# Kernel optimization log

Measured on AMD Instinct MI355X. Metric: run time of the kernel, lower is better.

Reference implementation:

```python
import jax, jax.numpy as jnp
import numpy as np

VOCAB, EMBED, HIDDEN, NCLS, PAD = 50257, 512, 1024, 4, 0

def setup_inputs() -> dict:
    key = jax.random.key(0)
    k1, k2, k3, k4, k5, k6 = jax.random.split(key, 6)
    emb = jax.random.uniform(k1, (VOCAB, EMBED), jnp.float32, -0.1, 0.1)
    emb = emb.at[PAD].set(0.0)
    W = jax.random.normal(k2, (HIDDEN, EMBED), jnp.float32) * (2.0 / (EMBED + HIDDEN)) ** 0.5
    b_w = jnp.zeros((HIDDEN,), jnp.float32)
    U = jax.random.normal(k3, (HIDDEN, HIDDEN), jnp.float32) * (1.0 / HIDDEN) ** 0.5
    V = jax.random.normal(k4, (NCLS, HIDDEN), jnp.float32) * (2.0 / (HIDDEN + NCLS)) ** 0.5
    b_v = jnp.zeros((NCLS,), jnp.float32)
    x = jax.random.randint(k5, (64, 512), 0, VOCAB, jnp.int32)
    return {"x": x, "emb": emb, "W": W, "b_w": b_w, "U": U, "V": V, "b_v": b_v}

def reference(x, emb, W, b_w, U, V, b_v):
    # x: [B, S] int tokens. Dropouts are identity (eval mode).
    embedded = emb[x]                      # [B, S, E]
    # Precompute Wx for all timesteps in one GEMM: [B, S, H]
    wx = jnp.einsum('bse,he->bsh', embedded, W) + b_w
    B = x.shape[0]
    h0 = jnp.zeros((B, W.shape[0]), embedded.dtype)

    def step(h, wx_t):
        h = jnp.tanh(wx_t + h @ U.T)       # [B, H]
        return h, None

    h_final, _ = jax.lax.scan(step, h0, jnp.swapaxes(wx, 0, 1))  # scan over S
    return h_final @ V.T + b_v             # [B, NCLS]
```

## Files before the change

### kernel.cpp

```cpp
#include <hip/hip_runtime.h>
#include <stdint.h>

#define B 64
#define S 512
#define E 512
#define H 1024
#define NCLS 4

typedef __attribute__((ext_vector_type(8))) short short8;
typedef __attribute__((ext_vector_type(4))) float f32x4;

__device__ __forceinline__ unsigned short f32_to_bf16(float f) {
    unsigned int x = __float_as_uint(f);
    unsigned int r = (x + 0x7fffu + ((x >> 16) & 1u)) >> 16;
    return (unsigned short)r;
}
__device__ __forceinline__ float bf16_to_f32(unsigned short u) {
    return __uint_as_float(((unsigned int)u) << 16);
}

__device__ __forceinline__ void store_sc4u(unsigned int* p, unsigned int v) {
    asm volatile("global_store_dword %0, %1, off sc0 sc1"
                 :: "v"(p), "v"(v) : "memory");
}

#define K1_LDA 40

__global__ __launch_bounds__(256) void k_wx_gemm(
    const int* __restrict__ x, const float* __restrict__ emb,
    const float* __restrict__ W, const float* __restrict__ bw,
    unsigned short* __restrict__ wx)
{
    __shared__ unsigned short Asub[128 * K1_LDA];
    __shared__ unsigned short Bsub[128 * K1_LDA];

    const int t  = threadIdx.x;
    const int mt = blockIdx.x;
    const int nt = blockIdx.y;
    const int i0 = mt * 128;
    const int j0 = nt * 128;

    const int r  = t >> 1;
    const int kh = (t & 1) * 16;
    const int tok = x[i0 + r];
    const float* arow = emb + (size_t)tok * E;
    const float* brow = W + (size_t)(j0 + r) * E;

    const int lane = t & 63;
    const int w    = t >> 6;
    const int wm   = (w >> 1) * 64;
    const int wn   = (w & 1) * 64;
    const int fr   = lane & 15;
    const int kg   = lane >> 4;

    f32x4 acc[4][4] = {};

    for (int kt = 0; kt < E; kt += 32) {
        __syncthreads();
        {
            union { unsigned short us[8]; uint4 v; } p;
            const float* srcA = arow + kt + kh;
            #pragma unroll
            for (int i = 0; i < 8; ++i) p.us[i] = f32_to_bf16(srcA[i]);
            *(uint4*)&Asub[r * K1_LDA + kh] = p.v;
            #pragma unroll
            for (int i = 0; i < 8; ++i) p.us[i] = f32_to_bf16(srcA[8 + i]);
            *(uint4*)&Asub[r * K1_LDA + kh + 8] = p.v;
            const float* srcB = brow + kt + kh;
            #pragma unroll
            for (int i = 0; i < 8; ++i) p.us[i] = f32_to_bf16(srcB[i]);
            *(uint4*)&Bsub[r * K1_LDA + kh] = p.v;
            #pragma unroll
            for (int i = 0; i < 8; ++i) p.us[i] = f32_to_bf16(srcB[8 + i]);
            *(uint4*)&Bsub[r * K1_LDA + kh + 8] = p.v;
        }
        __syncthreads();

        short8 a[4], b[4];
        #pragma unroll
        for (int mi = 0; mi < 4; ++mi)
            a[mi] = *(const short8*)&Asub[(wm + mi * 16 + fr) * K1_LDA + kg * 8];
        #pragma unroll
        for (int ni = 0; ni < 4; ++ni)
            b[ni] = *(const short8*)&Bsub[(wn + ni * 16 + fr) * K1_LDA + kg * 8];
        #pragma unroll
        for (int mi = 0; mi < 4; ++mi)
            #pragma unroll
            for (int ni = 0; ni < 4; ++ni)
                acc[mi][ni] = __builtin_amdgcn_mfma_f32_16x16x32_bf16(
                                  a[mi], b[ni], acc[mi][ni], 0, 0, 0);
    }

    float bwv[4];
    #pragma unroll
    for (int ni = 0; ni < 4; ++ni) bwv[ni] = bw[j0 + wn + ni * 16 + fr];
    #pragma unroll
    for (int mi = 0; mi < 4; ++mi) {
        #pragma unroll
        for (int ni = 0; ni < 4; ++ni) {
            const int gn = j0 + wn + ni * 16 + fr;
            #pragma unroll
            for (int rr = 0; rr < 4; ++rr) {
                const int gm = i0 + wm + mi * 16 + kg * 4 + rr;
                const int bb = gm >> 9;
                const int ss = gm & 511;
                wx[(size_t)(ss * B + bb) * H + gn] =
                    f32_to_bf16(acc[mi][ni][rr] + bwv[ni]);
            }
        }
    }
}

__global__ __launch_bounds__(256) void k_rnn(
    const unsigned short* __restrict__ wx, const float* __restrict__ U,
    const float* __restrict__ Vw, const float* __restrict__ bv,
    unsigned int* __restrict__ hbuf, unsigned int* __restrict__ flags,
    float* __restrict__ out)
{
    __shared__ __align__(16) unsigned short Uhi[32 * 1024];
    __shared__ __align__(16) unsigned short Ulo[32 * 1024];
    __shared__ __align__(16) unsigned short Hhi[8 * 1024];
    __shared__ __align__(16) unsigned short Hlo[8 * 1024];

    const int t   = threadIdx.x;
    const int g   = blockIdx.x & 7;
    const int m   = blockIdx.x >> 3;
    const int j0  = m * 32;
    const int bg0 = g * 8;

    for (int rr = 0; rr < 32; ++rr) {
        f32x4 v = *(const f32x4*)(U + (size_t)(j0 + rr) * H + t * 4);
        unsigned short h0 = f32_to_bf16(v[0]);
        unsigned short h1 = f32_to_bf16(v[1]);
        unsigned short h2 = f32_to_bf16(v[2]);
        unsigned short h3 = f32_to_bf16(v[3]);
        unsigned short l0 = f32_to_bf16(v[0] - bf16_to_f32(h0));
        unsigned short l1 = f32_to_bf16(v[1] - bf16_to_f32(h1));
        unsigned short l2 = f32_to_bf16(v[2] - bf16_to_f32(h2));
        unsigned short l3 = f32_to_bf16(v[3] - bf16_to_f32(h3));
        uint2 hwd, lwd;
        hwd.x = h0 | ((unsigned)h1 << 16); hwd.y = h2 | ((unsigned)h3 << 16);
        lwd.x = l0 | ((unsigned)l1 << 16); lwd.y = l2 | ((unsigned)l3 << 16);
        const int byteoff = (rr * 2048 + t * 8) ^ ((rr & 7) << 4);
        *(uint2*)((char*)Uhi + byteoff) = hwd;
        *(uint2*)((char*)Ulo + byteoff) = lwd;
    }

    const int lane  = t & 63;
    const int w     = t >> 6;
    const int fr    = lane & 15;
    const int kg    = lane >> 4;
    const int kbase = w * 256;
    const int abrow = fr & 7;
    const int ob    = t >> 5;
    const int oj    = t & 31;

    unsigned int* fl = flags + g * 32;
    float* redC = (float*)Hhi;
    unsigned int* Hh32 = (unsigned int*)Hhi;
    unsigned int* Hl32 = (unsigned int*)Hlo;

    float wxv = bf16_to_f32(wx[(size_t)(bg0 + ob) * H + j0 + oj]);

    __syncthreads();

    for (int ts = 0; ts < S; ++ts) {
        const unsigned int* hr = hbuf + (ts & 1) * (B * H);
        unsigned int*       hw = hbuf + ((ts + 1) & 1) * (B * H);

        if (t < 32)
            while (__hip_atomic_load(&fl[t], __ATOMIC_RELAXED,
                                     __HIP_MEMORY_SCOPE_AGENT) < (unsigned)ts) {}
        __syncthreads();

        float wx_next = 0.f;
        if (ts + 1 < S)
            wx_next = bf16_to_f32(wx[(size_t)((ts + 1) * B + bg0 + ob) * H + j0 + oj]);

        {
            const unsigned long long* src =
                (const unsigned long long*)(hr + (size_t)(bg0 + ob) * H);
            unsigned long long vv[16];
            #pragma unroll
            for (int i = 0; i < 16; ++i)
                vv[i] = __hip_atomic_load(src + oj + 32 * i, __ATOMIC_RELAXED,
                                          __HIP_MEMORY_SCOPE_AGENT);
            #pragma unroll
            for (int i = 0; i < 16; ++i) {
                const unsigned int v0 = (unsigned int)vv[i];
                const unsigned int v1 = (unsigned int)(vv[i] >> 32);
                const unsigned int hiw = (v0 >> 16) | (v1 & 0xffff0000u);
                const unsigned int low = (v0 & 0xffffu) | (v1 << 16);
                const int idx = (ob * 512 + oj + 32 * i) ^ (ob << 2);
                Hh32[idx] = hiw;
                Hl32[idx] = low;
            }
        }
        __syncthreads();

        f32x4 acc0 = {}, acc1 = {};
        #pragma unroll
        for (int kk = 0; kk < 8; ++kk) {
            const int k  = kbase + kk * 32 + kg * 8;
            const int ab = (abrow * 2048 + k * 2) ^ (abrow << 4);
            const short8 ahi = *(const short8*)((const char*)Hhi + ab);
            const short8 alo = *(const short8*)((const char*)Hlo + ab);
            const int b0 = (fr * 2048 + k * 2) ^ ((fr & 7) << 4);
            const int b1 = ((16 + fr) * 2048 + k * 2) ^ ((fr & 7) << 4);
            const short8 bhi0 = *(const short8*)((const char*)Uhi + b0);
            const short8 blo0 = *(const short8*)((const char*)Ulo + b0);
            const short8 bhi1 = *(const short8*)((const char*)Uhi + b1);
            const short8 blo1 = *(const short8*)((const char*)Ulo + b1);
            acc0 = __builtin_amdgcn_mfma_f32_16x16x32_bf16(ahi, bhi0, acc0, 0, 0, 0);
            acc0 = __builtin_amdgcn_mfma_f32_16x16x32_bf16(ahi, blo0, acc0, 0, 0, 0);
            acc0 = __builtin_amdgcn_mfma_f32_16x16x32_bf16(alo, bhi0, acc0, 0, 0, 0);
            acc1 = __builtin_amdgcn_mfma_f32_16x16x32_bf16(ahi, bhi1, acc1, 0, 0, 0);
            acc1 = __builtin_amdgcn_mfma_f32_16x16x32_bf16(ahi, blo1, acc1, 0, 0, 0);
            acc1 = __builtin_amdgcn_mfma_f32_16x16x32_bf16(alo, bhi1, acc1, 0, 0, 0);
        }
        __syncthreads();

        if (kg < 2) {
            #pragma unroll
            for (int rr = 0; rr < 4; ++rr) {
                const int mb = kg * 4 + rr;
                redC[w * 256 + mb * 32 + fr]      = acc0[rr];
                redC[w * 256 + mb * 32 + 16 + fr] = acc1[rr];
            }
        }
        __syncthreads();

        float sum = redC[       ob * 32 + oj] + redC[256 + ob * 32 + oj]
                  + redC[512 + ob * 32 + oj] + redC[768 + ob * 32 + oj];

        float p = wxv + sum;
        p = fminf(fmaxf(p, -15.f), 15.f);
        const float e  = __expf(2.0f * p);
        const float hv = 1.0f - 2.0f / (e + 1.0f);

        const unsigned short hib = f32_to_bf16(hv);
        const unsigned short lob = f32_to_bf16(hv - bf16_to_f32(hib));
        const unsigned int pk = ((unsigned int)hib << 16) | lob;
        store_sc4u(hw + (size_t)(bg0 + ob) * H + j0 + oj, pk);
        asm volatile("s_waitcnt vmcnt(0)" ::: "memory");
        __syncthreads();
        if (t == 0)
            __hip_atomic_store(&fl[m], (unsigned)(ts + 1), __ATOMIC_RELAXED,
                               __HIP_MEMORY_SCOPE_AGENT);
        wxv = wx_next;
    }

    if (m == 0) {
        if (t < 32)
            while (__hip_atomic_load(&fl[t], __ATOMIC_RELAXED,
                                     __HIP_MEMORY_SCOPE_AGENT) < (unsigned)S) {}
        __syncthreads();
        const unsigned int* hf = hbuf;
        const int o = t & 31, part = t >> 5;
        const int pb = o >> 2, c = o & 3;
        const unsigned long long* hrow =
            (const unsigned long long*)(hf + (size_t)(bg0 + pb) * H) + part * 64;
        const float* vrow = Vw + (size_t)c * H + part * 128;
        float partial = 0.f;
        for (int q = 0; q < 64; ++q) {
            unsigned long long vv = __hip_atomic_load(hrow + q, __ATOMIC_RELAXED,
                                                      __HIP_MEMORY_SCOPE_AGENT);
            const unsigned int v0 = (unsigned int)vv;
            const unsigned int v1 = (unsigned int)(vv >> 32);
            const float h0 = bf16_to_f32((unsigned short)(v0 >> 16))
                           + bf16_to_f32((unsigned short)(v0 & 0xffffu));
            const float h1 = bf16_to_f32((unsigned short)(v1 >> 16))
                           + bf16_to_f32((unsigned short)(v1 & 0xffffu));
            partial += h0 * vrow[2 * q] + h1 * vrow[2 * q + 1];
        }
        __syncthreads();
        redC[part * 32 + o] = partial;
        __syncthreads();
        if (t < 32) {
            float sv = 0.f;
            #pragma unroll
            for (int pq = 0; pq < 8; ++pq) sv += redC[pq * 32 + t];
            out[(bg0 + (t >> 2)) * NCLS + (t & 3)] = sv + bv[t & 3];
        }
    }
}

extern "C" void kernel_launch(void* const* d_in, const int* in_sizes, int n_in,
                              void* d_out, int out_size, void* d_ws, size_t ws_size,
                              hipStream_t stream)
{
    const int*   x   = (const int*)d_in[0];
    const float* emb = (const float*)d_in[1];
    const float* W   = (const float*)d_in[2];
    const float* bw  = (const float*)d_in[3];
    const float* U   = (const float*)d_in[4];
    const float* V   = (const float*)d_in[5];
    const float* bv  = (const float*)d_in[6];
    float* out = (float*)d_out;

    unsigned short* wx = (unsigned short*)d_ws;
    const size_t WX_BYTES = (size_t)S * B * H * sizeof(unsigned short);
    unsigned int* hbuf = (unsigned int*)((char*)d_ws + WX_BYTES);
    const size_t HB_BYTES = (size_t)2 * B * H * sizeof(unsigned int);
    unsigned int* flags = (unsigned int*)((char*)d_ws + WX_BYTES + HB_BYTES);

    hipMemsetAsync((char*)d_ws + WX_BYTES, 0, HB_BYTES + 1024, stream);

    hipLaunchKernelGGL(k_wx_gemm, dim3(256, 8), dim3(256), 0, stream,
                       x, emb, W, bw, wx);
    hipLaunchKernelGGL(k_rnn, dim3(256), dim3(256), 0, stream,
                       wx, U, V, bv, hbuf, flags, out);
}
```

Baseline: 1.871 ms.

## Replace per-step flag barrier with parity-tagged hidden state and drop U low split

Removes the per-block flag array and its spin-wait. Each stored hidden value now carries a parity tag in its low mantissa bit, and consumers spin directly on the data they load. This drops the store-drain wait and one barrier from every step of the serial recurrence. Separately, U is now kept only as a bf16 high part, which drops a third of the MFMAs and the Ulo shared buffer. That lowers the precision of the U product and slightly corrupts the low bit of the lo half of h.

```diff
diff --git a/kernel.cpp b/kernel.cpp
--- a/kernel.cpp
+++ b/kernel.cpp
@@ -114,11 +114,9 @@
 __global__ __launch_bounds__(256) void k_rnn(
     const unsigned short* __restrict__ wx, const float* __restrict__ U,
     const float* __restrict__ Vw, const float* __restrict__ bv,
-    unsigned int* __restrict__ hbuf, unsigned int* __restrict__ flags,
-    float* __restrict__ out)
+    unsigned int* __restrict__ hbuf, float* __restrict__ out)
 {
     __shared__ __align__(16) unsigned short Uhi[32 * 1024];
-    __shared__ __align__(16) unsigned short Ulo[32 * 1024];
     __shared__ __align__(16) unsigned short Hhi[8 * 1024];
     __shared__ __align__(16) unsigned short Hlo[8 * 1024];
 
@@ -130,20 +128,11 @@
 
     for (int rr = 0; rr < 32; ++rr) {
         f32x4 v = *(const f32x4*)(U + (size_t)(j0 + rr) * H + t * 4);
-        unsigned short h0 = f32_to_bf16(v[0]);
-        unsigned short h1 = f32_to_bf16(v[1]);
-        unsigned short h2 = f32_to_bf16(v[2]);
-        unsigned short h3 = f32_to_bf16(v[3]);
-        unsigned short l0 = f32_to_bf16(v[0] - bf16_to_f32(h0));
-        unsigned short l1 = f32_to_bf16(v[1] - bf16_to_f32(h1));
-        unsigned short l2 = f32_to_bf16(v[2] - bf16_to_f32(h2));
-        unsigned short l3 = f32_to_bf16(v[3] - bf16_to_f32(h3));
-        uint2 hwd, lwd;
-        hwd.x = h0 | ((unsigned)h1 << 16); hwd.y = h2 | ((unsigned)h3 << 16);
-        lwd.x = l0 | ((unsigned)l1 << 16); lwd.y = l2 | ((unsigned)l3 << 16);
+        uint2 hwd;
+        hwd.x = f32_to_bf16(v[0]) | ((unsigned)f32_to_bf16(v[1]) << 16);
+        hwd.y = f32_to_bf16(v[2]) | ((unsigned)f32_to_bf16(v[3]) << 16);
         const int byteoff = (rr * 2048 + t * 8) ^ ((rr & 7) << 4);
         *(uint2*)((char*)Uhi + byteoff) = hwd;
-        *(uint2*)((char*)Ulo + byteoff) = lwd;
     }
 
     const int lane  = t & 63;
@@ -155,7 +144,6 @@
     const int ob    = t >> 5;
     const int oj    = t & 31;
 
-    unsigned int* fl = flags + g * 32;
     float* redC = (float*)Hhi;
     unsigned int* Hh32 = (unsigned int*)Hhi;
     unsigned int* Hl32 = (unsigned int*)Hlo;
@@ -167,34 +155,32 @@
     for (int ts = 0; ts < S; ++ts) {
         const unsigned int* hr = hbuf + (ts & 1) * (B * H);
         unsigned int*       hw = hbuf + ((ts + 1) & 1) * (B * H);
-
-        if (t < 32)
-            while (__hip_atomic_load(&fl[t], __ATOMIC_RELAXED,
-                                     __HIP_MEMORY_SCOPE_AGENT) < (unsigned)ts) {}
-        __syncthreads();
+        const unsigned int exp  = ((unsigned)(ts + 1) >> 1) & 1u;
+        const unsigned int ptag = ((unsigned)(ts + 2) >> 1) & 1u;
+
+        const unsigned long long* src =
+            (const unsigned long long*)(hr + (size_t)(bg0 + ob) * H);
+        unsigned long long vv[16];
+        #pragma unroll
+        for (int i = 0; i < 16; ++i)
+            vv[i] = __hip_atomic_load(src + oj + 32 * i, __ATOMIC_RELAXED,
+                                      __HIP_MEMORY_SCOPE_AGENT);
 
         float wx_next = 0.f;
         if (ts + 1 < S)
             wx_next = bf16_to_f32(wx[(size_t)((ts + 1) * B + bg0 + ob) * H + j0 + oj]);
 
-        {
-            const unsigned long long* src =
-                (const unsigned long long*)(hr + (size_t)(bg0 + ob) * H);
-            unsigned long long vv[16];
-            #pragma unroll
-            for (int i = 0; i < 16; ++i)
+        #pragma unroll
+        for (int i = 0; i < 16; ++i) {
+            while ((((unsigned int)vv[i] ^ exp) |
+                    ((unsigned int)(vv[i] >> 32) ^ exp)) & 1u)
                 vv[i] = __hip_atomic_load(src + oj + 32 * i, __ATOMIC_RELAXED,
                                           __HIP_MEMORY_SCOPE_AGENT);
-            #pragma unroll
-            for (int i = 0; i < 16; ++i) {
-                const unsigned int v0 = (unsigned int)vv[i];
-                const unsigned int v1 = (unsigned int)(vv[i] >> 32);
-                const unsigned int hiw = (v0 >> 16) | (v1 & 0xffff0000u);
-                const unsigned int low = (v0 & 0xffffu) | (v1 << 16);
-                const int idx = (ob * 512 + oj + 32 * i) ^ (ob << 2);
-                Hh32[idx] = hiw;
-                Hl32[idx] = low;
-            }
+            const unsigned int v0 = (unsigned int)vv[i];
+            const unsigned int v1 = (unsigned int)(vv[i] >> 32);
+            const int idx = (ob * 512 + oj + 32 * i) ^ (ob << 2);
+            Hh32[idx] = (v0 >> 16) | (v1 & 0xffff0000u);
+            Hl32[idx] = (v0 & 0xffffu) | (v1 << 16);
         }
         __syncthreads();
 
@@ -208,14 +194,10 @@
             const int b0 = (fr * 2048 + k * 2) ^ ((fr & 7) << 4);
             const int b1 = ((16 + fr) * 2048 + k * 2) ^ ((fr & 7) << 4);
             const short8 bhi0 = *(const short8*)((const char*)Uhi + b0);
-            const short8 blo0 = *(const short8*)((const char*)Ulo + b0);
             const short8 bhi1 = *(const short8*)((const char*)Uhi + b1);
-            const short8 blo1 = *(const short8*)((const char*)Ulo + b1);
             acc0 = __builtin_amdgcn_mfma_f32_16x16x32_bf16(ahi, bhi0, acc0, 0, 0, 0);
-            acc0 = __builtin_amdgcn_mfma_f32_16x16x32_bf16(ahi, blo0, acc0, 0, 0, 0);
             acc0 = __builtin_amdgcn_mfma_f32_16x16x32_bf16(alo, bhi0, acc0, 0, 0, 0);
             acc1 = __builtin_amdgcn_mfma_f32_16x16x32_bf16(ahi, bhi1, acc1, 0, 0, 0);
-            acc1 = __builtin_amdgcn_mfma_f32_16x16x32_bf16(ahi, blo1, acc1, 0, 0, 0);
             acc1 = __builtin_amdgcn_mfma_f32_16x16x32_bf16(alo, bhi1, acc1, 0, 0, 0);
         }
         __syncthreads();
@@ -230,7 +212,7 @@
         }
         __syncthreads();
 
-        float sum = redC[       ob * 32 + oj] + redC[256 + ob * 32 + oj]
+        float sum = redC[      ob * 32 + oj] + redC[256 + ob * 32 + oj]
                   + redC[512 + ob * 32 + oj] + redC[768 + ob * 32 + oj];
 
         float p = wxv + sum;
@@ -240,21 +222,16 @@
 
         const unsigned short hib = f32_to_bf16(hv);
         const unsigned short lob = f32_to_bf16(hv - bf16_to_f32(hib));
-        const unsigned int pk = ((unsigned int)hib << 16) | lob;
+        unsigned int pk = ((unsigned int)hib << 16) | lob;
+        pk = (pk & ~1u) | ptag;
         store_sc4u(hw + (size_t)(bg0 + ob) * H + j0 + oj, pk);
-        asm volatile("s_waitcnt vmcnt(0)" ::: "memory");
-        __syncthreads();
-        if (t == 0)
-            __hip_atomic_store(&fl[m], (unsigned)(ts + 1), __ATOMIC_RELAXED,
-                               __HIP_MEMORY_SCOPE_AGENT);
+
+        __syncthreads();
         wxv = wx_next;
     }
 
     if (m == 0) {
-        if (t < 32)
-            while (__hip_atomic_load(&fl[t], __ATOMIC_RELAXED,
-                                     __HIP_MEMORY_SCOPE_AGENT) < (unsigned)S) {}
-        __syncthreads();
+        const unsigned int expf_ = ((unsigned)(S + 1) >> 1) & 1u;
         const unsigned int* hf = hbuf;
         const int o = t & 31, part = t >> 5;
         const int pb = o >> 2, c = o & 3;
@@ -263,10 +240,14 @@
         const float* vrow = Vw + (size_t)c * H + part * 128;
         float partial = 0.f;
         for (int q = 0; q < 64; ++q) {
-            unsigned long long vv = __hip_atomic_load(hrow + q, __ATOMIC_RELAXED,
-                                                      __HIP_MEMORY_SCOPE_AGENT);
-            const unsigned int v0 = (unsigned int)vv;
-            const unsigned int v1 = (unsigned int)(vv >> 32);
+            unsigned long long vvq = __hip_atomic_load(hrow + q, __ATOMIC_RELAXED,
+                                                       __HIP_MEMORY_SCOPE_AGENT);
+            while ((((unsigned int)vvq ^ expf_) |
+                    ((unsigned int)(vvq >> 32) ^ expf_)) & 1u)
+                vvq = __hip_atomic_load(hrow + q, __ATOMIC_RELAXED,
+                                        __HIP_MEMORY_SCOPE_AGENT);
+            const unsigned int v0 = (unsigned int)vvq;
+            const unsigned int v1 = (unsigned int)(vvq >> 32);
             const float h0 = bf16_to_f32((unsigned short)(v0 >> 16))
                            + bf16_to_f32((unsigned short)(v0 & 0xffffu));
             const float h1 = bf16_to_f32((unsigned short)(v1 >> 16))
@@ -302,12 +283,11 @@
     const size_t WX_BYTES = (size_t)S * B * H * sizeof(unsigned short);
     unsigned int* hbuf = (unsigned int*)((char*)d_ws + WX_BYTES);
     const size_t HB_BYTES = (size_t)2 * B * H * sizeof(unsigned int);
-    unsigned int* flags = (unsigned int*)((char*)d_ws + WX_BYTES + HB_BYTES);
-
-    hipMemsetAsync((char*)d_ws + WX_BYTES, 0, HB_BYTES + 1024, stream);
+
+    hipMemsetAsync((char*)d_ws + WX_BYTES, 0, HB_BYTES, stream);
 
     hipLaunchKernelGGL(k_wx_gemm, dim3(256, 8), dim3(256), 0, stream,
                        x, emb, W, bw, wx);
     hipLaunchKernelGGL(k_rnn, dim3(256), dim3(256), 0, stream,
-                       wx, U, V, bv, hbuf, flags, out);
-}
+                       wx, U, V, bv, hbuf, out);
+}
```

New measurement: 2.143 ms. 1.15x slower.
